# Performance work log

Hardware: AMD Instinct MI355X
Metric: run time of the kernel (lower is better)

The kernel has to match this reference:

```python
import jax, jax.numpy as jnp
import numpy as np

NEG = 0.01  # LeakyReLU negative_slope
N_NODES = 100000
N_EDGES = 400000
D = 128
IN_CH = 16
EDGE_DIM = 1


def _linear(x, w, b):
    # torch.nn.Linear convention: y = x @ W^T + b, W: [out, in]
    return x @ w.T + b


def setup_inputs() -> dict:
    key = jax.random.key(0)
    ks = jax.random.split(key, 32)

    def W(k, o, i):
        return jax.random.normal(k, (o, i), dtype=jnp.float32) * 0.02

    def B(k, o):
        return jax.random.normal(k, (o,), dtype=jnp.float32) * 0.02

    return {
        "x": jax.random.normal(ks[0], (N_NODES, IN_CH), dtype=jnp.float32),
        "edge_index": jax.random.randint(ks[1], (2, N_EDGES), 0, N_NODES, dtype=jnp.int64),
        "edge_weight": jax.random.uniform(ks[2], (N_EDGES, EDGE_DIM), dtype=jnp.float32),
        # prep MLP: in_ch -> 128 (LeakyReLU) -> 128 (Tanh)
        "prep_w0": W(ks[3], D, IN_CH), "prep_b0": B(ks[4], D),
        "prep_w1": W(ks[5], D, D), "prep_b1": B(ks[6], D),
        # GINEConv edge lin: edge_dim -> 128
        "edge_w": W(ks[7], D, EDGE_DIM), "edge_b": B(ks[8], D),
        # GINEConv nn: 128 -> 128 (LReLU) -> 128 (LReLU) -> 128 (Tanh)
        "mlp_w0": W(ks[9], D, D), "mlp_b0": B(ks[10], D),
        "mlp_w1": W(ks[11], D, D), "mlp_b1": B(ks[12], D),
        "mlp_w2": W(ks[13], D, D), "mlp_b2": B(ks[14], D),
        # post MLP: (128+128) -> 128 (LReLU) -> 64 (Tanh)
        "post_w0": W(ks[15], D, 2 * D), "post_b0": B(ks[16], D),
        "post_w1": W(ks[17], 64, D), "post_b1": B(ks[18], 64),
    }


def reference(x, edge_index, edge_weight,
              prep_w0, prep_b0, prep_w1, prep_b1,
              edge_w, edge_b,
              mlp_w0, mlp_b0, mlp_w1, mlp_b1, mlp_w2, mlp_b2,
              post_w0, post_b0, post_w1, post_b1):
    lrelu = lambda v: jax.nn.leaky_relu(v, negative_slope=NEG)
    n = x.shape[0]

    # sequential_prep
    h = lrelu(_linear(x, prep_w0, prep_b0))
    h = jnp.tanh(_linear(h, prep_w1, prep_b1))  # [N, D]

    r = h  # skip connection (x.clone())

    # GINEConv: message = relu(x_j + lin(edge_attr)); aggr = sum per dst
    e = _linear(edge_weight, edge_w, edge_b)            # [E, D]
    m = jax.nn.relu(h[edge_index[0]] + e)               # gather + edge add
    agg = jax.ops.segment_sum(m, edge_index[1], num_segments=n)  # scatter-sum
    z = h + agg  # (1 + eps) * x_i + aggr, eps = 0
    z = lrelu(_linear(z, mlp_w0, mlp_b0))
    z = lrelu(_linear(z, mlp_w1, mlp_b1))
    z = jnp.tanh(_linear(z, mlp_w2, mlp_b2))            # [N, D]

    # skip-cat
    h2 = jnp.concatenate([z, r], axis=1)                # [N, 2D]

    # sequential_post
    o = lrelu(_linear(h2, post_w0, post_b0))
    o = jnp.tanh(_linear(o, post_w1, post_b1))          # [N, 64]
    return o
```

## Files before the change

### kernel.cpp

```cpp
#include <hip/hip_runtime.h>

typedef short bf16x8 __attribute__((ext_vector_type(8)));
typedef float f32x4 __attribute__((ext_vector_type(4)));

#define NEG 0.01f

#define OFF_P0  0
#define OFF_P1  8192
#define OFF_M0  40960
#define OFF_Q0A 139264
#define OFF_Q0B 172032
#define OFF_Q1  204800
#define WBF_BYTES 221184

#define VMCNT0 asm volatile("s_waitcnt vmcnt(0)" ::: "memory")

__device__ __forceinline__ unsigned short f2bf(float f) {
  union { float f; unsigned u; } v; v.f = f;
  unsigned u = v.u;
  return (unsigned short)((u + 0x7fffu + ((u >> 16) & 1u)) >> 16);
}
__device__ __forceinline__ unsigned pack2(float a, float b) {
  return ((unsigned)f2bf(b) << 16) | (unsigned)f2bf(a);
}
__device__ __forceinline__ float bflo(unsigned u) { return __uint_as_float(u << 16); }
__device__ __forceinline__ float bfhi(unsigned u) { return __uint_as_float(u & 0xffff0000u); }
__device__ __forceinline__ float lrelu(float v) { return fmaxf(v, 0.0f) + NEG * fminf(v, 0.0f); }
__device__ __forceinline__ float tanh_fast(float x) {
  float e = __expf(2.0f * x);
  return 1.0f - __fdividef(2.0f, e + 1.0f);
}

__device__ __forceinline__ void gll16(const void* g, void* l) {
  __builtin_amdgcn_global_load_lds((const __attribute__((address_space(1))) void*)g,
                                   (__attribute__((address_space(3))) void*)l, 16, 0, 0);
}

__device__ __forceinline__ void gll_lin(const char* g, char* l, int nchunks, int wv, int nw, int lane) {
  for (int j = wv; j < nchunks; j += nw)
    gll16(g + j * 1024 + lane * 16, l + j * 1024 + lane * 16);
}

__device__ __forceinline__ void gll_rows(const char* gsrc, char* scr, int strip, int N, int lane) {
  #pragma unroll
  for (int c = 0; c < 8; ++c) {
    int L = c * 1024 + lane * 16;
    int row = strip + (L >> 8);
    row = row < N ? row : N - 1;
    gll16(gsrc + (size_t)row * 256 + (L & 255), scr + c * 1024 + lane * 16);
  }
}

__device__ __forceinline__ void copy_rows_out(const char* scr, char* gdst, int strip, int N, int lane) {
  #pragma unroll
  for (int c = 0; c < 8; ++c) {
    int L = c * 1024 + lane * 16;
    int row = strip + (L >> 8);
    if (row < N) *(uint4*)(gdst + (size_t)strip * 256 + L) = *(const uint4*)(scr + L);
  }
}

__device__ __forceinline__ void zacc82(f32x4 acc[8][2]) {
  #pragma unroll
  for (int m = 0; m < 8; ++m)
    #pragma unroll
    for (int n = 0; n < 2; ++n) { f32x4 z = {0.f,0.f,0.f,0.f}; acc[m][n] = z; }
}

__device__ __forceinline__ void gemm128(const char* wbase, const bf16x8 b[2][4],
                                        f32x4 acc[8][2], int l15, int lg) {
  __builtin_amdgcn_s_setprio(1);
  #pragma unroll
  for (int ks = 0; ks < 4; ++ks)
    #pragma unroll
    for (int mf = 0; mf < 8; ++mf) {
      const int row = 16*mf + l15;
      bf16x8 a = *(const bf16x8*)(wbase + row*256 + ((16*lg + 64*ks) ^ ((row&7)<<4)));
      acc[mf][0] = __builtin_amdgcn_mfma_f32_16x16x32_bf16(a, b[0][ks], acc[mf][0], 0,0,0);
      acc[mf][1] = __builtin_amdgcn_mfma_f32_16x16x32_bf16(a, b[1][ks], acc[mf][1], 0,0,0);
    }
  __builtin_amdgcn_s_setprio(0);
}

__device__ __forceinline__ void read_bfrags(const char* scr, bf16x8 b[2][4], int l15, int lg) {
  #pragma unroll
  for (int nf = 0; nf < 2; ++nf) {
    const int n = 16*nf + l15;
    #pragma unroll
    for (int ks = 0; ks < 4; ++ks)
      b[nf][ks] = *(const bf16x8*)(scr + n*256 + ((16*lg + 64*ks) ^ ((n&7)<<4)));
  }
}

template<int ACT>
__device__ __forceinline__ void ep_lds(const f32x4 acc[8][2], const float* __restrict__ bias,
                                       char* scr, int l15, int lg) {
  #pragma unroll
  for (int mf = 0; mf < 8; ++mf) {
    const int ch4 = 16*mf + 4*lg;
    const float4 bv = *(const float4*)(bias + ch4);
    #pragma unroll
    for (int nf = 0; nf < 2; ++nf) {
      const int n = 16*nf + l15;
      float v0 = acc[mf][nf][0]+bv.x, v1 = acc[mf][nf][1]+bv.y;
      float v2 = acc[mf][nf][2]+bv.z, v3 = acc[mf][nf][3]+bv.w;
      if (ACT == 0) { v0=lrelu(v0); v1=lrelu(v1); v2=lrelu(v2); v3=lrelu(v3); }
      else { v0=tanh_fast(v0); v1=tanh_fast(v1); v2=tanh_fast(v2); v3=tanh_fast(v3); }
      uint2 o = { pack2(v0,v1), pack2(v2,v3) };
      *(uint2*)(scr + n*256 + ((32*mf + 8*lg) ^ ((n&7)<<4))) = o;
    }
  }
}

extern "C" __global__ void __launch_bounds__(256) wpack_kernel(
    const float* __restrict__ pw0, const float* __restrict__ pw1,
    const float* __restrict__ mw0, const float* __restrict__ mw1, const float* __restrict__ mw2,
    const float* __restrict__ qw0, const float* __restrict__ qw1,
    char* wbf, int* deg, int N) {
  int gid = blockIdx.x * 256 + threadIdx.x;
  if (gid < 13824) {
    int c = gid;
    const float* src = nullptr;
    int dstB = 0;
    bool zero = false;
    if (c < 512) { int r = c >> 2, q = c & 3;
      dstB = OFF_P0 + r*64 + ((q*16) ^ ((r&3)<<4));
      if (q < 2) src = pw0 + r*16 + q*8; else zero = true;
    } else if (c < 2560) { int i = c - 512, r = i >> 4, q = i & 15;
      dstB = OFF_P1 + r*256 + ((q*16) ^ ((r&7)<<4));
      src = pw1 + r*128 + q*8;
    } else if (c < 8704) { int i = c - 2560, sl = i >> 11, j = i & 2047, r = j >> 4, q = j & 15;
      const float* m = (sl==0) ? mw0 : ((sl==1) ? mw1 : mw2);
      dstB = OFF_M0 + sl*32768 + r*256 + ((q*16) ^ ((r&7)<<4));
      src = m + r*128 + q*8;
    } else if (c < 10752) { int i = c - 8704, r = i >> 4, q = i & 15;
      dstB = OFF_Q0A + r*256 + ((q*16) ^ ((r&7)<<4));
      src = qw0 + r*256 + q*8;
    } else if (c < 12800) { int i = c - 10752, r = i >> 4, q = i & 15;
      dstB = OFF_Q0B + r*256 + ((q*16) ^ ((r&7)<<4));
      src = qw0 + r*256 + 128 + q*8;
    } else { int i = c - 12800, r = i >> 4, q = i & 15;
      dstB = OFF_Q1 + r*256 + ((q*16) ^ ((r&7)<<4));
      src = qw1 + r*128 + q*8;
    }
    ushort4 lo, hi;
    if (zero) { lo.x=lo.y=lo.z=lo.w=0; hi.x=hi.y=hi.z=hi.w=0; }
    else {
      float4 a = *(const float4*)src, b = *(const float4*)(src + 4);
      lo.x=f2bf(a.x); lo.y=f2bf(a.y); lo.z=f2bf(a.z); lo.w=f2bf(a.w);
      hi.x=f2bf(b.x); hi.y=f2bf(b.y); hi.z=f2bf(b.z); hi.w=f2bf(b.w);
    }
    *(ushort4*)(wbf + dstB) = lo;
    *(ushort4*)(wbf + dstB + 8) = hi;
  }
  if (gid < N) deg[gid] = 0;
}

extern "C" __global__ void __launch_bounds__(256, 2) prep_kernel(
    const float* __restrict__ x,
    const float* __restrict__ pb0, const float* __restrict__ pb1,
    const char* __restrict__ wbf,
    const int* __restrict__ ei, int* deg, int E,
    char* hB, int N) {
  __shared__ char wP[40960];
  __shared__ char scr_all[4 * 8192];
  const int tid = threadIdx.x, lane = tid & 63, wv = tid >> 6;
  const int l15 = lane & 15, lg = lane >> 4;

  gll_lin(wbf + OFF_P0, wP, 40, wv, 4, lane);
  for (int e = blockIdx.x*256 + tid; e < E; e += gridDim.x*256)
    atomicAdd(&deg[ei[E + e]], 1);
  VMCNT0; __syncthreads();
  char* scr = scr_all + wv * 8192;

  const int strip = blockIdx.x*128 + wv*32;
  if (strip >= N) return;

  bf16x8 bx[2];
  #pragma unroll
  for (int nf = 0; nf < 2; ++nf) {
    int node = strip + 16*nf + l15; node = node < N ? node : N-1;
    if (lg < 2) {
      float4 u = *(const float4*)(x + (size_t)node*16 + lg*8);
      float4 v = *(const float4*)(x + (size_t)node*16 + lg*8 + 4);
      bf16x8 t;
      t[0]=(short)f2bf(u.x); t[1]=(short)f2bf(u.y); t[2]=(short)f2bf(u.z); t[3]=(short)f2bf(u.w);
      t[4]=(short)f2bf(v.x); t[5]=(short)f2bf(v.y); t[6]=(short)f2bf(v.z); t[7]=(short)f2bf(v.w);
      bx[nf] = t;
    } else {
      bf16x8 t = {0,0,0,0,0,0,0,0}; bx[nf] = t;
    }
  }
  f32x4 acc[8][2];
  zacc82(acc);
  __builtin_amdgcn_s_setprio(1);
  #pragma unroll
  for (int mf = 0; mf < 8; ++mf) {
    const int row = 16*mf + l15;
    bf16x8 a = *(const bf16x8*)(wP + row*64 + ((16*lg) ^ ((row&3)<<4)));
    acc[mf][0] = __builtin_amdgcn_mfma_f32_16x16x32_bf16(a, bx[0], acc[mf][0], 0,0,0);
    acc[mf][1] = __builtin_amdgcn_mfma_f32_16x16x32_bf16(a, bx[1], acc[mf][1], 0,0,0);
  }
  __builtin_amdgcn_s_setprio(0);
  ep_lds<0>(acc, pb0, scr, l15, lg);
  bf16x8 b1[2][4];
  read_bfrags(scr, b1, l15, lg);
  zacc82(acc);
  gemm128(wP + 8192, b1, acc, l15, lg);
  ep_lds<1>(acc, pb1, scr, l15, lg);
  copy_rows_out(scr, hB, strip, N, lane);
}

extern "C" __global__ void __launch_bounds__(256) scan_partials_kernel(
    const int* __restrict__ deg, int* partials, int N) {
  __shared__ int red[256];
  int b = blockIdx.x, t = threadIdx.x;
  int base = b * 2048 + t * 8, s = 0;
  #pragma unroll
  for (int i = 0; i < 8; ++i) { int idx = base + i; s += (idx < N) ? deg[idx] : 0; }
  red[t] = s; __syncthreads();
  for (int off = 128; off > 0; off >>= 1) {
    if (t < off) red[t] += red[t + off];
    __syncthreads();
  }
  if (t == 0) partials[b] = red[0];
}

extern "C" __global__ void __launch_bounds__(256) scan_apply_kernel(
    const int* __restrict__ deg, const int* __restrict__ partials,
    int* offs, int* cur, int N, int nb) {
  __shared__ int sc[256];
  __shared__ int baseSh;
  int b = blockIdx.x, t = threadIdx.x;
  if (t < 64) {
    int v = (t < b && t < nb) ? partials[t] : 0;
    #pragma unroll
    for (int off = 32; off > 0; off >>= 1) v += __shfl_xor(v, off);
    if (t == 0) baseSh = v;
  }
  int base = b * 2048 + t * 8;
  int loc[8], s = 0;
  #pragma unroll
  for (int i = 0; i < 8; ++i) { int idx = base + i; loc[i] = (idx < N) ? deg[idx] : 0; s += loc[i]; }
  sc[t] = s; __syncthreads();
  for (int off = 1; off < 256; off <<= 1) {
    int v = sc[t];
    int u = (t >= off) ? sc[t - off] : 0;
    __syncthreads();
    sc[t] = v + u;
    __syncthreads();
  }
  int run = baseSh + ((t == 0) ? 0 : sc[t - 1]);
  #pragma unroll
  for (int i = 0; i < 8; ++i) {
    int idx = base + i;
    if (idx < N) { offs[idx] = run; cur[idx] = run; run += loc[i]; }
  }
}

extern "C" __global__ void __launch_bounds__(256) scatter_kernel(
    const int* __restrict__ ei, const float* __restrict__ ew,
    int* cur, int2* recs, int E) {
  int e = blockIdx.x * 256 + threadIdx.x;
  if (e < E) {
    int dst = ei[E + e];
    int slot = atomicAdd(&cur[dst], 1);
    int2 r; r.x = ei[e]; r.y = __float_as_int(ew[e]);
    recs[slot] = r;
  }
}

extern "C" __global__ void __launch_bounds__(256) agg_kernel(
    const int* __restrict__ offs, const int* __restrict__ cur,
    const int2* __restrict__ recs,
    const float* __restrict__ elw, const float* __restrict__ elb,
    const char* __restrict__ hB, char* zB, int N) {
  const int lane = threadIdx.x & 63, wv = threadIdx.x >> 6;
  const int half = lane >> 5, l31 = lane & 31;
  const int node = blockIdx.x * 8 + wv * 2 + half;
  if (node >= N) return;
  const float4 wl = *(const float4*)(elw + 4*l31);
  const float4 bl = *(const float4*)(elb + 4*l31);
  const int byteL = l31 * 8;
  const int s = offs[node], e = cur[node];
  float c0 = 0.f, c1 = 0.f, c2 = 0.f, c3 = 0.f;
  int j = s;
  for (; j + 2 <= e; j += 2) {
    int2 r0 = recs[j], r1 = recs[j+1];
    uint2 u0 = *(const uint2*)(hB + (size_t)r0.x*256 + (byteL ^ ((r0.x&7)<<4)));
    uint2 u1 = *(const uint2*)(hB + (size_t)r1.x*256 + (byteL ^ ((r1.x&7)<<4)));
    float w0 = __int_as_float(r0.y), w1 = __int_as_float(r1.y);
    c0 += fmaxf(bflo(u0.x) + w0*wl.x + bl.x, 0.f);
    c1 += fmaxf(bfhi(u0.x) + w0*wl.y + bl.y, 0.f);
    c2 += fmaxf(bflo(u0.y) + w0*wl.z + bl.z, 0.f);
    c3 += fmaxf(bfhi(u0.y) + w0*wl.w + bl.w, 0.f);
    c0 += fmaxf(bflo(u1.x) + w1*wl.x + bl.x, 0.f);
    c1 += fmaxf(bfhi(u1.x) + w1*wl.y + bl.y, 0.f);
    c2 += fmaxf(bflo(u1.y) + w1*wl.z + bl.z, 0.f);
    c3 += fmaxf(bfhi(u1.y) + w1*wl.w + bl.w, 0.f);
  }
  if (j < e) {
    int2 r = recs[j];
    uint2 u = *(const uint2*)(hB + (size_t)r.x*256 + (byteL ^ ((r.x&7)<<4)));
    float w = __int_as_float(r.y);
    c0 += fmaxf(bflo(u.x) + w*wl.x + bl.x, 0.f);
    c1 += fmaxf(bfhi(u.x) + w*wl.y + bl.y, 0.f);
    c2 += fmaxf(bflo(u.y) + w*wl.z + bl.z, 0.f);
    c3 += fmaxf(bfhi(u.y) + w*wl.w + bl.w, 0.f);
  }
  const int swz = byteL ^ ((node&7)<<4);
  uint2 hs = *(const uint2*)(hB + (size_t)node*256 + swz);
  uint2 o;
  o.x = pack2(bflo(hs.x) + c0, bfhi(hs.x) + c1);
  o.y = pack2(bflo(hs.y) + c2, bfhi(hs.y) + c3);
  *(uint2*)(zB + (size_t)node*256 + swz) = o;
}

extern "C" __global__ void __launch_bounds__(448) nodeA_kernel(
    const char* __restrict__ zB, const char* __restrict__ wbf,
    const float* __restrict__ mb0, const float* __restrict__ mb1, const float* __restrict__ mb2,
    char* z3, int N, int ntiles) {
  __shared__ char wM[98304];
  __shared__ char scr_all[7 * 8192];
  const int tid = threadIdx.x, lane = tid & 63, wv = tid >> 6;
  const int l15 = lane & 15, lg = lane >> 4;

  gll_lin(wbf + OFF_M0, wM, 96, wv, 7, lane);
  VMCNT0; __syncthreads();
  char* scr = scr_all + wv * 8192;

  for (int tile = blockIdx.x; tile < ntiles; tile += gridDim.x) {
    const int strip = tile*224 + wv*32;
    if (strip >= N) continue;
    gll_rows(zB, scr, strip, N, lane);
    VMCNT0;
    bf16x8 b0[2][4];
    read_bfrags(scr, b0, l15, lg);
    f32x4 acc[8][2];
    zacc82(acc);
    gemm128(wM, b0, acc, l15, lg);
    ep_lds<0>(acc, mb0, scr, l15, lg);
    bf16x8 b1[2][4];
    read_bfrags(scr, b1, l15, lg);
    zacc82(acc);
    gemm128(wM + 32768, b1, acc, l15, lg);
    ep_lds<0>(acc, mb1, scr, l15, lg);
    bf16x8 b2[2][4];
    read_bfrags(scr, b2, l15, lg);
    zacc82(acc);
    gemm128(wM + 65536, b2, acc, l15, lg);
    ep_lds<1>(acc, mb2, scr, l15, lg);
    copy_rows_out(scr, z3, strip, N, lane);
  }
}

extern "C" __global__ void __launch_bounds__(512) nodeB_kernel(
    const char* __restrict__ z3, const char* hB, const char* __restrict__ wbf,
    const float* __restrict__ qb0, const float* __restrict__ qb1,
    float* out, int N, int ntiles) {
  __shared__ char wQ[81920];
  __shared__ char scr_all[8 * 8192];
  const int tid = threadIdx.x, lane = tid & 63, wv = tid >> 6;
  const int l15 = lane & 15, lg = lane >> 4;

  gll_lin(wbf + OFF_Q0A, wQ, 80, wv, 8, lane);
  VMCNT0; __syncthreads();
  char* scr = scr_all + wv * 8192;

  for (int tile = blockIdx.x; tile < ntiles; tile += gridDim.x) {
    const int strip = tile*256 + wv*32;
    if (strip >= N) continue;
    gll_rows(z3, scr, strip, N, lane);
    bf16x8 bh[2][4];
    #pragma unroll
    for (int nf = 0; nf < 2; ++nf) {
      int node = strip + 16*nf + l15; node = node < N ? node : N-1;
      const char* hr = hB + (size_t)node*256;
      const int sw = (node&7) << 4;
      #pragma unroll
      for (int ks = 0; ks < 4; ++ks)
        bh[nf][ks] = *(const bf16x8*)(hr + ((16*lg + 64*ks) ^ sw));
    }
    VMCNT0;
    bf16x8 bz[2][4];
    read_bfrags(scr, bz, l15, lg);
    f32x4 acc[8][2];
    zacc82(acc);
    gemm128(wQ, bz, acc, l15, lg);
    gemm128(wQ + 32768, bh, acc, l15, lg);
    ep_lds<0>(acc, qb0, scr, l15, lg);

    bf16x8 bt[2][4];
    read_bfrags(scr, bt, l15, lg);
    f32x4 a2[4][2];
    #pragma unroll
    for (int m = 0; m < 4; ++m)
      #pragma unroll
      for (int n = 0; n < 2; ++n) { f32x4 z = {0.f,0.f,0.f,0.f}; a2[m][n] = z; }
    __builtin_amdgcn_s_setprio(1);
    #pragma unroll
    for (int ks = 0; ks < 4; ++ks)
      #pragma unroll
      for (int mf = 0; mf < 4; ++mf) {
        const int row = 16*mf + l15;
        bf16x8 a = *(const bf16x8*)(wQ + 65536 + row*256 + ((16*lg + 64*ks) ^ ((row&7)<<4)));
        a2[mf][0] = __builtin_amdgcn_mfma_f32_16x16x32_bf16(a, bt[0][ks], a2[mf][0], 0,0,0);
        a2[mf][1] = __builtin_amdgcn_mfma_f32_16x16x32_bf16(a, bt[1][ks], a2[mf][1], 0,0,0);
      }
    __builtin_amdgcn_s_setprio(0);
    #pragma unroll
    for (int mf = 0; mf < 4; ++mf) {
      const int ch4 = 16*mf + 4*lg;
      const float4 bv = *(const float4*)(qb1 + ch4);
      #pragma unroll
      for (int nf = 0; nf < 2; ++nf) {
        const int node = strip + 16*nf + l15;
        if (node < N) {
          float4 o;
          o.x = tanh_fast(a2[mf][nf][0] + bv.x);
          o.y = tanh_fast(a2[mf][nf][1] + bv.y);
          o.z = tanh_fast(a2[mf][nf][2] + bv.z);
          o.w = tanh_fast(a2[mf][nf][3] + bv.w);
          *(float4*)(out + (size_t)node*64 + ch4) = o;
        }
      }
    }
  }
}

extern "C" void kernel_launch(void* const* d_in, const int* in_sizes, int n_in,
                              void* d_out, int out_size, void* d_ws, size_t ws_size,
                              hipStream_t stream) {
  const float* x   = (const float*)d_in[0];
  const int*   ei  = (const int*)d_in[1];
  const float* ew  = (const float*)d_in[2];
  const float* pw0 = (const float*)d_in[3];
  const float* pb0 = (const float*)d_in[4];
  const float* pw1 = (const float*)d_in[5];
  const float* pb1 = (const float*)d_in[6];
  const float* elw = (const float*)d_in[7];
  const float* elb = (const float*)d_in[8];
  const float* mw0 = (const float*)d_in[9];
  const float* mb0 = (const float*)d_in[10];
  const float* mw1 = (const float*)d_in[11];
  const float* mb1 = (const float*)d_in[12];
  const float* mw2 = (const float*)d_in[13];
  const float* mb2 = (const float*)d_in[14];
  const float* qw0 = (const float*)d_in[15];
  const float* qb0 = (const float*)d_in[16];
  const float* qw1 = (const float*)d_in[17];
  const float* qb1 = (const float*)d_in[18];
  float* out = (float*)d_out;

  const int N = in_sizes[0] / 16;
  const int E = in_sizes[1] / 2;

  char* p = (char*)d_ws;
  auto alloc = [&](size_t bytes) { char* r = p; p += (bytes + 255) & ~(size_t)255; return r; };
  const size_t rowBytes = (size_t)N * 256;

  char* zB      = alloc(rowBytes);
  char* z3      = alloc(rowBytes);
  int2* recs    = (int2*)alloc((size_t)E * 8);
  int*  deg     = (int*)alloc((size_t)N * 4);
  int*  offs    = (int*)alloc((size_t)N * 4);
  int*  cur     = (int*)alloc((size_t)N * 4);
  int*  part    = (int*)alloc(256 * 4);
  char* wbf     = alloc(WBF_BYTES);

  char* hB;
  if ((size_t)(p - (char*)d_ws) + rowBytes <= ws_size) {
    hB = alloc(rowBytes);
  } else {
    hB = (char*)d_out;
  }

  const int pblk    = (N + 127) / 128;
  const int ntilesA = (N + 223) / 224;
  const int ntilesB = (N + 255) / 256;
  const int nb1  = (N + 2047) / 2048;
  const int eblk = (E + 255) / 256;
  const int pgrid = ((13824 > N ? 13824 : N) + 255) / 256;

  wpack_kernel<<<dim3(pgrid), dim3(256), 0, stream>>>(pw0, pw1, mw0, mw1, mw2, qw0, qw1,
                                                      wbf, deg, N);
  prep_kernel<<<dim3(pblk), dim3(256), 0, stream>>>(x, pb0, pb1, wbf, ei, deg, E, hB, N);
  scan_partials_kernel<<<dim3(nb1), dim3(256), 0, stream>>>(deg, part, N);
  scan_apply_kernel<<<dim3(nb1), dim3(256), 0, stream>>>(deg, part, offs, cur, N, nb1);
  scatter_kernel<<<dim3(eblk), dim3(256), 0, stream>>>(ei, ew, cur, recs, E);
  agg_kernel<<<dim3((N + 7) / 8), dim3(256), 0, stream>>>(offs, cur, recs, elw, elb, hB, zB, N);
  nodeA_kernel<<<dim3(256), dim3(448), 0, stream>>>(zB, wbf, mb0, mb1, mb2, z3, N, ntilesA);
  nodeB_kernel<<<dim3(256), dim3(512), 0, stream>>>(z3, hB, wbf, qb0, qb1, out, N, ntilesB);
}
```

Before: 244.1 us.

## Merge pipeline into one cooperative persistent kernel with grid-wide syncs

Replaces the eight separate launches (weight pack, prep MLP with degree count, two-pass scan, scatter, aggregation, node MLP A, node MLP B) with a single cooperative kernel of 256 blocks by 448 threads. The stages are separated by grid.sync(), the scan is rebuilt as a per-block scan plus a single-block base scan, and the weights are staged through one shared LDS slab. The edge aggregation is fused into the node MLP A strip loop, so aggregated rows go straight to LDS and the zB intermediate buffer and its global round trip disappear. The goal is to remove launch gaps and one global buffer pass, at the cost of several grid barriers, a fixed one-block-per-CU occupancy, and fewer waves in flight to hide latency on the gather-heavy aggregation.

```diff
diff --git a/kernel.cpp b/kernel.cpp
--- a/kernel.cpp
+++ b/kernel.cpp
@@ -1,4 +1,7 @@
 #include <hip/hip_runtime.h>
+#include <hip/hip_cooperative_groups.h>
+
+namespace cg = cooperative_groups;
 
 typedef short bf16x8 __attribute__((ext_vector_type(8)));
 typedef float f32x4 __attribute__((ext_vector_type(4)));
@@ -13,7 +16,14 @@
 #define OFF_Q1  204800
 #define WBF_BYTES 221184
 
+#define NBLK 256
+#define NTHR 448
+#define NWAVE 7
+#define GSTRIDE (NBLK*NTHR)
+#define NWAVES_G (NBLK*NWAVE)
+
 #define VMCNT0 asm volatile("s_waitcnt vmcnt(0)" ::: "memory")
+#define LGKM0  asm volatile("s_waitcnt lgkmcnt(0)" ::: "memory")
 
 __device__ __forceinline__ unsigned short f2bf(float f) {
   union { float f; unsigned u; } v; v.f = f;
@@ -35,12 +45,10 @@
   __builtin_amdgcn_global_load_lds((const __attribute__((address_space(1))) void*)g,
                                    (__attribute__((address_space(3))) void*)l, 16, 0, 0);
 }
-
-__device__ __forceinline__ void gll_lin(const char* g, char* l, int nchunks, int wv, int nw, int lane) {
-  for (int j = wv; j < nchunks; j += nw)
+__device__ __forceinline__ void gll_lin(const char* g, char* l, int nchunks, int wvi, int lane) {
+  for (int j = wvi; j < nchunks; j += NWAVE)
     gll16(g + j * 1024 + lane * 16, l + j * 1024 + lane * 16);
 }
-
 __device__ __forceinline__ void gll_rows(const char* gsrc, char* scr, int strip, int N, int lane) {
   #pragma unroll
   for (int c = 0; c < 8; ++c) {
@@ -50,7 +58,6 @@
     gll16(gsrc + (size_t)row * 256 + (L & 255), scr + c * 1024 + lane * 16);
   }
 }
-
 __device__ __forceinline__ void copy_rows_out(const char* scr, char* gdst, int strip, int N, int lane) {
   #pragma unroll
   for (int c = 0; c < 8; ++c) {
@@ -59,14 +66,12 @@
     if (row < N) *(uint4*)(gdst + (size_t)strip * 256 + L) = *(const uint4*)(scr + L);
   }
 }
-
 __device__ __forceinline__ void zacc82(f32x4 acc[8][2]) {
   #pragma unroll
   for (int m = 0; m < 8; ++m)
     #pragma unroll
     for (int n = 0; n < 2; ++n) { f32x4 z = {0.f,0.f,0.f,0.f}; acc[m][n] = z; }
 }
-
 __device__ __forceinline__ void gemm128(const char* wbase, const bf16x8 b[2][4],
                                         f32x4 acc[8][2], int l15, int lg) {
   __builtin_amdgcn_s_setprio(1);
@@ -81,7 +86,6 @@
     }
   __builtin_amdgcn_s_setprio(0);
 }
-
 __device__ __forceinline__ void read_bfrags(const char* scr, bf16x8 b[2][4], int l15, int lg) {
   #pragma unroll
   for (int nf = 0; nf < 2; ++nf) {
@@ -91,7 +95,6 @@
       b[nf][ks] = *(const bf16x8*)(scr + n*256 + ((16*lg + 64*ks) ^ ((n&7)<<4)));
   }
 }
-
 template<int ACT>
 __device__ __forceinline__ void ep_lds(const f32x4 acc[8][2], const float* __restrict__ bias,
                                        char* scr, int l15, int lg) {
@@ -112,12 +115,29 @@
   }
 }
 
-extern "C" __global__ void __launch_bounds__(256) wpack_kernel(
-    const float* __restrict__ pw0, const float* __restrict__ pw1,
-    const float* __restrict__ mw0, const float* __restrict__ mw1, const float* __restrict__ mw2,
-    const float* __restrict__ qw0, const float* __restrict__ qw1,
-    char* wbf, int* deg, int N) {
-  int gid = blockIdx.x * 256 + threadIdx.x;
+extern "C" __global__ void __launch_bounds__(NTHR, 1) mega_kernel(
+    const float* __restrict__ x, const int* __restrict__ ei, const float* __restrict__ ew,
+    const float* __restrict__ pw0, const float* __restrict__ pb0,
+    const float* __restrict__ pw1, const float* __restrict__ pb1,
+    const float* __restrict__ elw, const float* __restrict__ elb,
+    const float* __restrict__ mw0, const float* __restrict__ mb0,
+    const float* __restrict__ mw1, const float* __restrict__ mb1,
+    const float* __restrict__ mw2, const float* __restrict__ mb2,
+    const float* __restrict__ qw0, const float* __restrict__ qb0,
+    const float* __restrict__ qw1, const float* __restrict__ qb1,
+    float* out, char* hB, char* z3, int2* recs,
+    int* deg, int* offs, int* cur, int* part, int* bases, char* wbf,
+    int N, int E, int S) {
+  __shared__ char wSlab[98304];
+  __shared__ char scr_all[NWAVE*8192];
+  cg::grid_group grid = cg::this_grid();
+  const int tid = threadIdx.x, lane = tid & 63, wv = tid >> 6;
+  const int l15 = lane & 15, lg = lane >> 4;
+  const int b = blockIdx.x;
+  const int gid = b*NTHR + tid;
+  const int gwave = b*NWAVE + wv;
+  char* scr = scr_all + wv*8192;
+
   if (gid < 13824) {
     int c = gid;
     const float* src = nullptr;
@@ -146,230 +166,166 @@
     ushort4 lo, hi;
     if (zero) { lo.x=lo.y=lo.z=lo.w=0; hi.x=hi.y=hi.z=hi.w=0; }
     else {
-      float4 a = *(const float4*)src, b = *(const float4*)(src + 4);
+      float4 a = *(const float4*)src, bb = *(const float4*)(src + 4);
       lo.x=f2bf(a.x); lo.y=f2bf(a.y); lo.z=f2bf(a.z); lo.w=f2bf(a.w);
-      hi.x=f2bf(b.x); hi.y=f2bf(b.y); hi.z=f2bf(b.z); hi.w=f2bf(b.w);
+      hi.x=f2bf(bb.x); hi.y=f2bf(bb.y); hi.z=f2bf(bb.z); hi.w=f2bf(bb.w);
     }
     *(ushort4*)(wbf + dstB) = lo;
     *(ushort4*)(wbf + dstB + 8) = hi;
   }
-  if (gid < N) deg[gid] = 0;
-}
-
-extern "C" __global__ void __launch_bounds__(256, 2) prep_kernel(
-    const float* __restrict__ x,
-    const float* __restrict__ pb0, const float* __restrict__ pb1,
-    const char* __restrict__ wbf,
-    const int* __restrict__ ei, int* deg, int E,
-    char* hB, int N) {
-  __shared__ char wP[40960];
-  __shared__ char scr_all[4 * 8192];
-  const int tid = threadIdx.x, lane = tid & 63, wv = tid >> 6;
-  const int l15 = lane & 15, lg = lane >> 4;
-
-  gll_lin(wbf + OFF_P0, wP, 40, wv, 4, lane);
-  for (int e = blockIdx.x*256 + tid; e < E; e += gridDim.x*256)
-    atomicAdd(&deg[ei[E + e]], 1);
+  for (int i = gid; i < N; i += GSTRIDE) deg[i] = 0;
+  __threadfence(); grid.sync();
+
+  gll_lin(wbf + OFF_P0, wSlab, 40, wv, lane);
+  for (int e = gid; e < E; e += GSTRIDE) atomicAdd(&deg[ei[E + e]], 1);
   VMCNT0; __syncthreads();
-  char* scr = scr_all + wv * 8192;
-
-  const int strip = blockIdx.x*128 + wv*32;
-  if (strip >= N) return;
-
-  bf16x8 bx[2];
-  #pragma unroll
-  for (int nf = 0; nf < 2; ++nf) {
-    int node = strip + 16*nf + l15; node = node < N ? node : N-1;
-    if (lg < 2) {
-      float4 u = *(const float4*)(x + (size_t)node*16 + lg*8);
-      float4 v = *(const float4*)(x + (size_t)node*16 + lg*8 + 4);
-      bf16x8 t;
-      t[0]=(short)f2bf(u.x); t[1]=(short)f2bf(u.y); t[2]=(short)f2bf(u.z); t[3]=(short)f2bf(u.w);
-      t[4]=(short)f2bf(v.x); t[5]=(short)f2bf(v.y); t[6]=(short)f2bf(v.z); t[7]=(short)f2bf(v.w);
-      bx[nf] = t;
-    } else {
-      bf16x8 t = {0,0,0,0,0,0,0,0}; bx[nf] = t;
-    }
-  }
-  f32x4 acc[8][2];
-  zacc82(acc);
-  __builtin_amdgcn_s_setprio(1);
-  #pragma unroll
-  for (int mf = 0; mf < 8; ++mf) {
-    const int row = 16*mf + l15;
-    bf16x8 a = *(const bf16x8*)(wP + row*64 + ((16*lg) ^ ((row&3)<<4)));
-    acc[mf][0] = __builtin_amdgcn_mfma_f32_16x16x32_bf16(a, bx[0], acc[mf][0], 0,0,0);
-    acc[mf][1] = __builtin_amdgcn_mfma_f32_16x16x32_bf16(a, bx[1], acc[mf][1], 0,0,0);
-  }
-  __builtin_amdgcn_s_setprio(0);
-  ep_lds<0>(acc, pb0, scr, l15, lg);
-  bf16x8 b1[2][4];
-  read_bfrags(scr, b1, l15, lg);
-  zacc82(acc);
-  gemm128(wP + 8192, b1, acc, l15, lg);
-  ep_lds<1>(acc, pb1, scr, l15, lg);
-  copy_rows_out(scr, hB, strip, N, lane);
-}
-
-extern "C" __global__ void __launch_bounds__(256) scan_partials_kernel(
-    const int* __restrict__ deg, int* partials, int N) {
-  __shared__ int red[256];
-  int b = blockIdx.x, t = threadIdx.x;
-  int base = b * 2048 + t * 8, s = 0;
-  #pragma unroll
-  for (int i = 0; i < 8; ++i) { int idx = base + i; s += (idx < N) ? deg[idx] : 0; }
-  red[t] = s; __syncthreads();
-  for (int off = 128; off > 0; off >>= 1) {
-    if (t < off) red[t] += red[t + off];
+  for (int s = gwave; s < S; s += NWAVES_G) {
+    const int strip = s*32;
+    bf16x8 bx[2];
+    #pragma unroll
+    for (int nf = 0; nf < 2; ++nf) {
+      int node = strip + 16*nf + l15; node = node < N ? node : N-1;
+      if (lg < 2) {
+        float4 u = *(const float4*)(x + (size_t)node*16 + lg*8);
+        float4 v = *(const float4*)(x + (size_t)node*16 + lg*8 + 4);
+        bf16x8 t;
+        t[0]=(short)f2bf(u.x); t[1]=(short)f2bf(u.y); t[2]=(short)f2bf(u.z); t[3]=(short)f2bf(u.w);
+        t[4]=(short)f2bf(v.x); t[5]=(short)f2bf(v.y); t[6]=(short)f2bf(v.z); t[7]=(short)f2bf(v.w);
+        bx[nf] = t;
+      } else {
+        bf16x8 t = {0,0,0,0,0,0,0,0}; bx[nf] = t;
+      }
+    }
+    f32x4 acc[8][2];
+    zacc82(acc);
+    __builtin_amdgcn_s_setprio(1);
+    #pragma unroll
+    for (int mf = 0; mf < 8; ++mf) {
+      const int row = 16*mf + l15;
+      bf16x8 a = *(const bf16x8*)(wSlab + row*64 + ((16*lg) ^ ((row&3)<<4)));
+      acc[mf][0] = __builtin_amdgcn_mfma_f32_16x16x32_bf16(a, bx[0], acc[mf][0], 0,0,0);
+      acc[mf][1] = __builtin_amdgcn_mfma_f32_16x16x32_bf16(a, bx[1], acc[mf][1], 0,0,0);
+    }
+    __builtin_amdgcn_s_setprio(0);
+    ep_lds<0>(acc, pb0, scr, l15, lg);
+    bf16x8 b1[2][4];
+    read_bfrags(scr, b1, l15, lg);
+    zacc82(acc);
+    gemm128(wSlab + 8192, b1, acc, l15, lg);
+    ep_lds<1>(acc, pb1, scr, l15, lg);
+    copy_rows_out(scr, hB, strip, N, lane);
+  }
+  __threadfence(); grid.sync();
+
+  int* sums = (int*)scr_all;
+  const int myDeg = (gid < N) ? deg[gid] : 0;
+  sums[tid] = myDeg; __syncthreads();
+  for (int off = 1; off < NTHR; off <<= 1) {
+    int v = sums[tid];
+    int u = (tid >= off) ? sums[tid - off] : 0;
     __syncthreads();
-  }
-  if (t == 0) partials[b] = red[0];
-}
-
-extern "C" __global__ void __launch_bounds__(256) scan_apply_kernel(
-    const int* __restrict__ deg, const int* __restrict__ partials,
-    int* offs, int* cur, int N, int nb) {
-  __shared__ int sc[256];
-  __shared__ int baseSh;
-  int b = blockIdx.x, t = threadIdx.x;
-  if (t < 64) {
-    int v = (t < b && t < nb) ? partials[t] : 0;
-    #pragma unroll
-    for (int off = 32; off > 0; off >>= 1) v += __shfl_xor(v, off);
-    if (t == 0) baseSh = v;
-  }
-  int base = b * 2048 + t * 8;
-  int loc[8], s = 0;
-  #pragma unroll
-  for (int i = 0; i < 8; ++i) { int idx = base + i; loc[i] = (idx < N) ? deg[idx] : 0; s += loc[i]; }
-  sc[t] = s; __syncthreads();
-  for (int off = 1; off < 256; off <<= 1) {
-    int v = sc[t];
-    int u = (t >= off) ? sc[t - off] : 0;
+    sums[tid] = v + u;
     __syncthreads();
-    sc[t] = v + u;
-    __syncthreads();
-  }
-  int run = baseSh + ((t == 0) ? 0 : sc[t - 1]);
-  #pragma unroll
-  for (int i = 0; i < 8; ++i) {
-    int idx = base + i;
-    if (idx < N) { offs[idx] = run; cur[idx] = run; run += loc[i]; }
-  }
-}
-
-extern "C" __global__ void __launch_bounds__(256) scatter_kernel(
-    const int* __restrict__ ei, const float* __restrict__ ew,
-    int* cur, int2* recs, int E) {
-  int e = blockIdx.x * 256 + threadIdx.x;
-  if (e < E) {
+  }
+  const int excl = sums[tid] - myDeg;
+  if (tid == NTHR-1) part[b] = sums[tid];
+  __threadfence(); grid.sync();
+  if (b == 0 && tid < 64) {
+    int p0 = part[4*tid], p1 = part[4*tid+1], p2 = part[4*tid+2], p3 = part[4*tid+3];
+    int tot = p0+p1+p2+p3, run = tot;
+    #pragma unroll
+    for (int off = 1; off < 64; off <<= 1) { int u = __shfl_up(run, off); if (tid >= off) run += u; }
+    int le = run - tot;
+    bases[4*tid]   = le;
+    bases[4*tid+1] = le + p0;
+    bases[4*tid+2] = le + p0 + p1;
+    bases[4*tid+3] = le + p0 + p1 + p2;
+  }
+  __threadfence(); grid.sync();
+  if (gid < N) { int o = bases[b] + excl; offs[gid] = o; cur[gid] = o; }
+  __threadfence(); grid.sync();
+
+  for (int e = gid; e < E; e += GSTRIDE) {
     int dst = ei[E + e];
     int slot = atomicAdd(&cur[dst], 1);
     int2 r; r.x = ei[e]; r.y = __float_as_int(ew[e]);
     recs[slot] = r;
   }
-}
-
-extern "C" __global__ void __launch_bounds__(256) agg_kernel(
-    const int* __restrict__ offs, const int* __restrict__ cur,
-    const int2* __restrict__ recs,
-    const float* __restrict__ elw, const float* __restrict__ elb,
-    const char* __restrict__ hB, char* zB, int N) {
-  const int lane = threadIdx.x & 63, wv = threadIdx.x >> 6;
-  const int half = lane >> 5, l31 = lane & 31;
-  const int node = blockIdx.x * 8 + wv * 2 + half;
-  if (node >= N) return;
-  const float4 wl = *(const float4*)(elw + 4*l31);
-  const float4 bl = *(const float4*)(elb + 4*l31);
-  const int byteL = l31 * 8;
-  const int s = offs[node], e = cur[node];
-  float c0 = 0.f, c1 = 0.f, c2 = 0.f, c3 = 0.f;
-  int j = s;
-  for (; j + 2 <= e; j += 2) {
-    int2 r0 = recs[j], r1 = recs[j+1];
-    uint2 u0 = *(const uint2*)(hB + (size_t)r0.x*256 + (byteL ^ ((r0.x&7)<<4)));
-    uint2 u1 = *(const uint2*)(hB + (size_t)r1.x*256 + (byteL ^ ((r1.x&7)<<4)));
-    float w0 = __int_as_float(r0.y), w1 = __int_as_float(r1.y);
-    c0 += fmaxf(bflo(u0.x) + w0*wl.x + bl.x, 0.f);
-    c1 += fmaxf(bfhi(u0.x) + w0*wl.y + bl.y, 0.f);
-    c2 += fmaxf(bflo(u0.y) + w0*wl.z + bl.z, 0.f);
-    c3 += fmaxf(bfhi(u0.y) + w0*wl.w + bl.w, 0.f);
-    c0 += fmaxf(bflo(u1.x) + w1*wl.x + bl.x, 0.f);
-    c1 += fmaxf(bfhi(u1.x) + w1*wl.y + bl.y, 0.f);
-    c2 += fmaxf(bflo(u1.y) + w1*wl.z + bl.z, 0.f);
-    c3 += fmaxf(bfhi(u1.y) + w1*wl.w + bl.w, 0.f);
-  }
-  if (j < e) {
-    int2 r = recs[j];
-    uint2 u = *(const uint2*)(hB + (size_t)r.x*256 + (byteL ^ ((r.x&7)<<4)));
-    float w = __int_as_float(r.y);
-    c0 += fmaxf(bflo(u.x) + w*wl.x + bl.x, 0.f);
-    c1 += fmaxf(bfhi(u.x) + w*wl.y + bl.y, 0.f);
-    c2 += fmaxf(bflo(u.y) + w*wl.z + bl.z, 0.f);
-    c3 += fmaxf(bfhi(u.y) + w*wl.w + bl.w, 0.f);
-  }
-  const int swz = byteL ^ ((node&7)<<4);
-  uint2 hs = *(const uint2*)(hB + (size_t)node*256 + swz);
-  uint2 o;
-  o.x = pack2(bflo(hs.x) + c0, bfhi(hs.x) + c1);
-  o.y = pack2(bflo(hs.y) + c2, bfhi(hs.y) + c3);
-  *(uint2*)(zB + (size_t)node*256 + swz) = o;
-}
-
-extern "C" __global__ void __launch_bounds__(448) nodeA_kernel(
-    const char* __restrict__ zB, const char* __restrict__ wbf,
-    const float* __restrict__ mb0, const float* __restrict__ mb1, const float* __restrict__ mb2,
-    char* z3, int N, int ntiles) {
-  __shared__ char wM[98304];
-  __shared__ char scr_all[7 * 8192];
-  const int tid = threadIdx.x, lane = tid & 63, wv = tid >> 6;
-  const int l15 = lane & 15, lg = lane >> 4;
-
-  gll_lin(wbf + OFF_M0, wM, 96, wv, 7, lane);
+  __threadfence(); grid.sync();
+
+  gll_lin(wbf + OFF_M0, wSlab, 96, wv, lane);
   VMCNT0; __syncthreads();
-  char* scr = scr_all + wv * 8192;
-
-  for (int tile = blockIdx.x; tile < ntiles; tile += gridDim.x) {
-    const int strip = tile*224 + wv*32;
-    if (strip >= N) continue;
-    gll_rows(zB, scr, strip, N, lane);
-    VMCNT0;
-    bf16x8 b0[2][4];
-    read_bfrags(scr, b0, l15, lg);
-    f32x4 acc[8][2];
-    zacc82(acc);
-    gemm128(wM, b0, acc, l15, lg);
-    ep_lds<0>(acc, mb0, scr, l15, lg);
-    bf16x8 b1[2][4];
-    read_bfrags(scr, b1, l15, lg);
-    zacc82(acc);
-    gemm128(wM + 32768, b1, acc, l15, lg);
-    ep_lds<0>(acc, mb1, scr, l15, lg);
-    bf16x8 b2[2][4];
-    read_bfrags(scr, b2, l15, lg);
-    zacc82(acc);
-    gemm128(wM + 65536, b2, acc, l15, lg);
-    ep_lds<1>(acc, mb2, scr, l15, lg);
-    copy_rows_out(scr, z3, strip, N, lane);
-  }
-}
-
-extern "C" __global__ void __launch_bounds__(512) nodeB_kernel(
-    const char* __restrict__ z3, const char* hB, const char* __restrict__ wbf,
-    const float* __restrict__ qb0, const float* __restrict__ qb1,
-    float* out, int N, int ntiles) {
-  __shared__ char wQ[81920];
-  __shared__ char scr_all[8 * 8192];
-  const int tid = threadIdx.x, lane = tid & 63, wv = tid >> 6;
-  const int l15 = lane & 15, lg = lane >> 4;
-
-  gll_lin(wbf + OFF_Q0A, wQ, 80, wv, 8, lane);
+  {
+    const int half = lane >> 5, l31 = lane & 31;
+    const int byteL = l31 * 8;
+    const float4 wl = *(const float4*)(elw + 4*l31);
+    const float4 bl = *(const float4*)(elb + 4*l31);
+    for (int s = gwave; s < S; s += NWAVES_G) {
+      const int strip = s*32;
+      for (int pr = 0; pr < 16; ++pr) {
+        const int lrow = 2*pr + half;
+        const int node = strip + lrow;
+        if (node < N) {
+          const int s0 = offs[node], e0 = cur[node];
+          float c0=0.f, c1=0.f, c2=0.f, c3=0.f;
+          int j = s0;
+          for (; j + 2 <= e0; j += 2) {
+            int2 r0 = recs[j], r1 = recs[j+1];
+            uint2 u0 = *(const uint2*)(hB + (size_t)r0.x*256 + (byteL ^ ((r0.x&7)<<4)));
+            uint2 u1 = *(const uint2*)(hB + (size_t)r1.x*256 + (byteL ^ ((r1.x&7)<<4)));
+            float w0 = __int_as_float(r0.y), w1 = __int_as_float(r1.y);
+            c0 += fmaxf(bflo(u0.x) + w0*wl.x + bl.x, 0.f);
+            c1 += fmaxf(bfhi(u0.x) + w0*wl.y + bl.y, 0.f);
+            c2 += fmaxf(bflo(u0.y) + w0*wl.z + bl.z, 0.f);
+            c3 += fmaxf(bfhi(u0.y) + w0*wl.w + bl.w, 0.f);
+            c0 += fmaxf(bflo(u1.x) + w1*wl.x + bl.x, 0.f);
+            c1 += fmaxf(bfhi(u1.x) + w1*wl.y + bl.y, 0.f);
+            c2 += fmaxf(bflo(u1.y) + w1*wl.z + bl.z, 0.f);
+            c3 += fmaxf(bfhi(u1.y) + w1*wl.w + bl.w, 0.f);
+          }
+          if (j < e0) {
+            int2 r = recs[j];
+            uint2 u = *(const uint2*)(hB + (size_t)r.x*256 + (byteL ^ ((r.x&7)<<4)));
+            float w = __int_as_float(r.y);
+            c0 += fmaxf(bflo(u.x) + w*wl.x + bl.x, 0.f);
+            c1 += fmaxf(bfhi(u.x) + w*wl.y + bl.y, 0.f);
+            c2 += fmaxf(bflo(u.y) + w*wl.z + bl.z, 0.f);
+            c3 += fmaxf(bfhi(u.y) + w*wl.w + bl.w, 0.f);
+          }
+          const int swz = byteL ^ ((lrow&7)<<4);
+          uint2 hs = *(const uint2*)(hB + (size_t)node*256 + swz);
+          uint2 o;
+          o.x = pack2(bflo(hs.x) + c0, bfhi(hs.x) + c1);
+          o.y = pack2(bflo(hs.y) + c2, bfhi(hs.y) + c3);
+          *(uint2*)(scr + lrow*256 + swz) = o;
+        }
+      }
+      LGKM0;
+      bf16x8 b0[2][4];
+      read_bfrags(scr, b0, l15, lg);
+      f32x4 acc[8][2];
+      zacc82(acc);
+      gemm128(wSlab, b0, acc, l15, lg);
+      ep_lds<0>(acc, mb0, scr, l15, lg);
+      bf16x8 b1f[2][4];
+      read_bfrags(scr, b1f, l15, lg);
+      zacc82(acc);
+      gemm128(wSlab + 32768, b1f, acc, l15, lg);
+      ep_lds<0>(acc, mb1, scr, l15, lg);
+      bf16x8 b2f[2][4];
+      read_bfrags(scr, b2f, l15, lg);
+      zacc82(acc);
+      gemm128(wSlab + 65536, b2f, acc, l15, lg);
+      ep_lds<1>(acc, mb2, scr, l15, lg);
+      copy_rows_out(scr, z3, strip, N, lane);
+    }
+  }
+  __threadfence(); grid.sync();
+
+  gll_lin(wbf + OFF_Q0A, wSlab, 80, wv, lane);
   VMCNT0; __syncthreads();
-  char* scr = scr_all + wv * 8192;
-
-  for (int tile = blockIdx.x; tile < ntiles; tile += gridDim.x) {
-    const int strip = tile*256 + wv*32;
-    if (strip >= N) continue;
+  for (int s = gwave; s < S; s += NWAVES_G) {
+    const int strip = s*32;
     gll_rows(z3, scr, strip, N, lane);
     bf16x8 bh[2][4];
     #pragma unroll
@@ -386,10 +342,9 @@
     read_bfrags(scr, bz, l15, lg);
     f32x4 acc[8][2];
     zacc82(acc);
-    gemm128(wQ, bz, acc, l15, lg);
-    gemm128(wQ + 32768, bh, acc, l15, lg);
+    gemm128(wSlab, bz, acc, l15, lg);
+    gemm128(wSlab + 32768, bh, acc, l15, lg);
     ep_lds<0>(acc, qb0, scr, l15, lg);
-
     bf16x8 bt[2][4];
     read_bfrags(scr, bt, l15, lg);
     f32x4 a2[4][2];
@@ -403,7 +358,7 @@
       #pragma unroll
       for (int mf = 0; mf < 4; ++mf) {
         const int row = 16*mf + l15;
-        bf16x8 a = *(const bf16x8*)(wQ + 65536 + row*256 + ((16*lg + 64*ks) ^ ((row&7)<<4)));
+        bf16x8 a = *(const bf16x8*)(wSlab + 65536 + row*256 + ((16*lg + 64*ks) ^ ((row&7)<<4)));
         a2[mf][0] = __builtin_amdgcn_mfma_f32_16x16x32_bf16(a, bt[0][ks], a2[mf][0], 0,0,0);
         a2[mf][1] = __builtin_amdgcn_mfma_f32_16x16x32_bf16(a, bt[1][ks], a2[mf][1], 0,0,0);
       }
@@ -452,20 +407,21 @@
   const float* qb1 = (const float*)d_in[18];
   float* out = (float*)d_out;
 
-  const int N = in_sizes[0] / 16;
-  const int E = in_sizes[1] / 2;
+  int N = in_sizes[0] / 16;
+  int E = in_sizes[1] / 2;
+  int S = (N + 31) / 32;
 
   char* p = (char*)d_ws;
   auto alloc = [&](size_t bytes) { char* r = p; p += (bytes + 255) & ~(size_t)255; return r; };
   const size_t rowBytes = (size_t)N * 256;
 
-  char* zB      = alloc(rowBytes);
   char* z3      = alloc(rowBytes);
   int2* recs    = (int2*)alloc((size_t)E * 8);
   int*  deg     = (int*)alloc((size_t)N * 4);
   int*  offs    = (int*)alloc((size_t)N * 4);
   int*  cur     = (int*)alloc((size_t)N * 4);
-  int*  part    = (int*)alloc(256 * 4);
+  int*  part    = (int*)alloc(NBLK * 4);
+  int*  bases   = (int*)alloc(NBLK * 4);
   char* wbf     = alloc(WBF_BYTES);
 
   char* hB;
@@ -475,20 +431,16 @@
     hB = (char*)d_out;
   }
 
-  const int pblk    = (N + 127) / 128;
-  const int ntilesA = (N + 223) / 224;
-  const int ntilesB = (N + 255) / 256;
-  const int nb1  = (N + 2047) / 2048;
-  const int eblk = (E + 255) / 256;
-  const int pgrid = ((13824 > N ? 13824 : N) + 255) / 256;
-
-  wpack_kernel<<<dim3(pgrid), dim3(256), 0, stream>>>(pw0, pw1, mw0, mw1, mw2, qw0, qw1,
-                                                      wbf, deg, N);
-  prep_kernel<<<dim3(pblk), dim3(256), 0, stream>>>(x, pb0, pb1, wbf, ei, deg, E, hB, N);
-  scan_partials_kernel<<<dim3(nb1), dim3(256), 0, stream>>>(deg, part, N);
-  scan_apply_kernel<<<dim3(nb1), dim3(256), 0, stream>>>(deg, part, offs, cur, N, nb1);
-  scatter_kernel<<<dim3(eblk), dim3(256), 0, stream>>>(ei, ew, cur, recs, E);
-  agg_kernel<<<dim3((N + 7) / 8), dim3(256), 0, stream>>>(offs, cur, recs, elw, elb, hB, zB, N);
-  nodeA_kernel<<<dim3(256), dim3(448), 0, stream>>>(zB, wbf, mb0, mb1, mb2, z3, N, ntilesA);
-  nodeB_kernel<<<dim3(256), dim3(512), 0, stream>>>(z3, hB, wbf, qb0, qb1, out, N, ntilesB);
-}
+  void* kargs[] = {
+    (void*)&x, (void*)&ei, (void*)&ew,
+    (void*)&pw0, (void*)&pb0, (void*)&pw1, (void*)&pb1,
+    (void*)&elw, (void*)&elb,
+    (void*)&mw0, (void*)&mb0, (void*)&mw1, (void*)&mb1, (void*)&mw2, (void*)&mb2,
+    (void*)&qw0, (void*)&qb0, (void*)&qw1, (void*)&qb1,
+    (void*)&out, (void*)&hB, (void*)&z3, (void*)&recs,
+    (void*)&deg, (void*)&offs, (void*)&cur, (void*)&part, (void*)&bases, (void*)&wbf,
+    (void*)&N, (void*)&E, (void*)&S
+  };
+  hipLaunchCooperativeKernel((const void*)mega_kernel, dim3(NBLK), dim3(NTHR),
+                             kargs, 0, stream);
+}
```

Result: slower. 809.5 us (+231.6%).
